# Kernel optimization log

Hardware: AMD Instinct MI355X
Metric: run time of the kernel (lower is better)

## Reference

```python
import jax, jax.numpy as jnp
import numpy as np

D_PET = 128
B = 16


def _mlp(k_vectors, W1, b1, W2, b2, W3, b3):
    # filter_calculator: Linear(3,d) -> silu -> Linear(d,d) -> silu -> Linear(d,d)
    x = jax.nn.silu(jnp.einsum('bkc,cd->bkd', k_vectors, W1) + b1)
    x = jax.nn.silu(jnp.einsum('bkd,de->bke', x, W2) + b2)
    return jnp.einsum('bkd,de->bke', x, W3) + b3


def setup_inputs() -> dict:
    key = jax.random.key(0)
    ks = jax.random.split(key, 10)
    N_B, N_k = 2048, 256
    k_vectors = jax.random.normal(ks[0], (B, N_k, 3), dtype=jnp.float32)
    positions = jax.random.normal(ks[1], (N_B, 3), dtype=jnp.float32)
    h = jax.random.normal(ks[2], (N_B, D_PET), dtype=jnp.float32)
    batch = jnp.sort(jax.random.randint(ks[3], (N_B,), 0, B))
    s3 = 1.0 / np.sqrt(3.0)
    sd = 1.0 / np.sqrt(D_PET)
    W1 = jax.random.uniform(ks[4], (3, D_PET), jnp.float32, -s3, s3)
    b1 = jnp.zeros((D_PET,), jnp.float32)
    W2 = jax.random.uniform(ks[5], (D_PET, D_PET), jnp.float32, -sd, sd)
    b2 = jnp.zeros((D_PET,), jnp.float32)
    W3 = jax.random.uniform(ks[6], (D_PET, D_PET), jnp.float32, -sd, sd)
    b3 = jnp.zeros((D_PET,), jnp.float32)
    return {"k_vectors": k_vectors, "positions": positions, "h": h,
            "W1": W1, "b1": b1, "W2": W2, "b2": b2, "W3": W3, "b3": b3,
            "batch": batch}


def reference(k_vectors, positions, h, W1, b1, W2, b2, W3, b3, batch):
    # gather per-atom k-vectors: [N_B, N_k, 3]
    kv = k_vectors[batch]
    # phase k . r : [N_B, N_k]
    phase = jnp.einsum('nc,nkc->nk', positions, kv)
    ikr = jnp.exp(1j * phase)  # complex64, [N_B, N_k]
    # s = segment-sum over atoms of exp(-i k.r) * h : [B, N_k, d_pet]
    contrib = jnp.conj(ikr)[:, :, None] * h[:, None, :]
    s = jax.ops.segment_sum(contrib, batch, num_segments=B)
    # filter values from k-vectors: [B, N_k, d_pet]
    filt = _mlp(k_vectors, W1, b1, W2, b2, W3, b3)
    # new h: sum over k of exp(i k.r) * s[batch] * filt[batch] : [N_B, d_pet]
    product = ikr[:, :, None] * s[batch] * filt[batch]
    return jnp.sum(product, axis=1)
```

## Files before the change

### kernel.cpp

```cpp
#include <hip/hip_runtime.h>
#include <math.h>

#define D_PET 128
#define NK    256
#define NB    2048
#define NBATCH 16

__device__ __forceinline__ float silu(float x) {
    return x / (1.0f + expf(-x));
}

__device__ __forceinline__ int lower_bound_dev(const int* a, int n, int v) {
    int lo = 0, hi = n;
    while (lo < hi) {
        int m = (lo + hi) >> 1;
        if (a[m] < v) lo = m + 1; else hi = m;
    }
    return lo;
}

#define S_BLOCKS 512
#define MJ 8

#define SLOAD(S, c0)                                                         \
    do {                                                                     \
        _Pragma("unroll")                                                    \
        for (int i_ = 0; i_ < 4; i_++) {                                     \
            int a_ = (c0) * 4 + i_;                                          \
            hb##S[i_] = *(const float4*)(hp + (size_t)(base + a_) * D_PET);  \
            cb##S[i_] = cs[a_ * 8 + kq];                                     \
        }                                                                    \
    } while (0)

#define SFMA(S)                                                              \
    do {                                                                     \
        _Pragma("unroll")                                                    \
        for (int i_ = 0; i_ < 4; i_++) {                                     \
            float4 hv = hb##S[i_]; float2 q = cb##S[i_];                     \
            re[0]=fmaf(q.x,hv.x,re[0]); im[0]=fmaf(-q.y,hv.x,im[0]);         \
            re[1]=fmaf(q.x,hv.y,re[1]); im[1]=fmaf(-q.y,hv.y,im[1]);         \
            re[2]=fmaf(q.x,hv.z,re[2]); im[2]=fmaf(-q.y,hv.z,im[2]);         \
            re[3]=fmaf(q.x,hv.w,re[3]); im[3]=fmaf(-q.y,hv.w,im[3]);         \
        }                                                                    \
    } while (0)

__global__ void __launch_bounds__(256) smlp_kernel(
                           const float* __restrict__ kvec,
                           const float* __restrict__ pos,
                           const float* __restrict__ h,
                           const int* __restrict__ batch,
                           const float* __restrict__ W1, const float* __restrict__ b1,
                           const float* __restrict__ W2, const float* __restrict__ b2,
                           const float* __restrict__ W3, const float* __restrict__ b3,
                           float* __restrict__ filt,
                           float* __restrict__ ts) {
    __shared__ float smem[24 + 2048];

    if (blockIdx.x < S_BLOCKS) {
        int bi = blockIdx.x;
        int v  = (bi & 7) * 64 + (bi >> 3);
        int b  = v >> 5;
        int kt = v & 31;
        int dq = threadIdx.x & 31;
        int kq = threadIdx.x >> 5;
        int k  = kt * 8 + kq;
        int d0 = dq * 4;

        float*  kv_s = smem;
        float2* cs   = (float2*)(smem + 24);

        if (threadIdx.x < 24)
            kv_s[threadIdx.x] = kvec[((size_t)b * NK + kt * 8) * 3 + threadIdx.x];

        int lo = lower_bound_dev(batch, NB, b);
        int hi = lower_bound_dev(batch, NB, b + 1);

        float re[4] = {0.f,0.f,0.f,0.f}, im[4] = {0.f,0.f,0.f,0.f};
        const float* hp = h + d0;

        for (int base = lo; base < hi; base += 128) {
            int m = hi - base; if (m > 128) m = 128;
            __syncthreads();
#pragma unroll
            for (int i = 0; i < 4; i++) {
                int p = threadIdx.x * 4 + i;
                int a = p >> 3, kk = p & 7;
                if (a < m) {
                    int n = base + a;
                    float ph = pos[n*3+0]*kv_s[kk*3+0]
                             + pos[n*3+1]*kv_s[kk*3+1]
                             + pos[n*3+2]*kv_s[kk*3+2];
                    float sv, cv; sincosf(ph, &sv, &cv);
                    cs[a * 8 + kk] = make_float2(cv, sv);
                }
            }
            __syncthreads();

            float4 hb0[4], hb1[4];
            float2 cb0[4], cb1[4];
            int nch = m >> 2;
            if (nch) {
                SLOAD(0, 0);
                int c = 1;
                for (; c + 1 < nch; c += 2) {
                    SLOAD(1, c);     __builtin_amdgcn_sched_barrier(0); SFMA(0);
                    SLOAD(0, c + 1); __builtin_amdgcn_sched_barrier(0); SFMA(1);
                }
                if (c < nch) {
                    SLOAD(1, c); __builtin_amdgcn_sched_barrier(0);
                    SFMA(0); SFMA(1);
                } else {
                    __builtin_amdgcn_sched_barrier(0); SFMA(0);
                }
            }
            for (int a = nch * 4; a < m; a++) {
                float4 hv = *(const float4*)(hp + (size_t)(base + a) * D_PET);
                float2 q  = cs[a * 8 + kq];
                re[0]=fmaf(q.x,hv.x,re[0]); im[0]=fmaf(-q.y,hv.x,im[0]);
                re[1]=fmaf(q.x,hv.y,re[1]); im[1]=fmaf(-q.y,hv.y,im[1]);
                re[2]=fmaf(q.x,hv.z,re[2]); im[2]=fmaf(-q.y,hv.z,im[2]);
                re[3]=fmaf(q.x,hv.w,re[3]); im[3]=fmaf(-q.y,hv.w,im[3]);
            }
        }

        size_t o = (((size_t)b * NK + k) * D_PET + d0) * 2;
        *(float4*)(ts + o)     = make_float4(re[0], im[0], re[1], im[1]);
        *(float4*)(ts + o + 4) = make_float4(re[2], im[2], re[3], im[3]);
        return;
    }

    int bk0 = (blockIdx.x - S_BLOCKS) * MJ;
    int d   = threadIdx.x & (D_PET - 1);
    int jg  = threadIdx.x >> 7;

    float* kv_s  = smem;
    float* x_lds = smem + 24;

    if (threadIdx.x < MJ * 3) kv_s[threadIdx.x] = kvec[bk0 * 3 + threadIdx.x];
    __syncthreads();

    float w10 = W1[0 * D_PET + d], w11 = W1[1 * D_PET + d], w12 = W1[2 * D_PET + d];
    float bb1 = b1[d];
    float4 x1;
    {
        float* xp = (float*)&x1;
#pragma unroll
        for (int i = 0; i < 4; i++) {
            int j = jg * 4 + i;
            float a = bb1;
            a = fmaf(kv_s[j * 3 + 0], w10, a);
            a = fmaf(kv_s[j * 3 + 1], w11, a);
            a = fmaf(kv_s[j * 3 + 2], w12, a);
            xp[i] = silu(a);
        }
    }
    *(float4*)&x_lds[(d << 3) + (jg << 2)] = x1;
    __syncthreads();

    float acc0 = b2[d], acc1 = acc0, acc2 = acc0, acc3 = acc0;
#pragma unroll
    for (int e0 = 0; e0 < D_PET; e0 += 8) {
        float w[8];
#pragma unroll
        for (int i = 0; i < 8; i++) w[i] = W2[(e0 + i) * D_PET + d];
        __builtin_amdgcn_sched_barrier(0);
#pragma unroll
        for (int i = 0; i < 8; i++) {
            float4 xv = *(const float4*)&x_lds[((e0 + i) << 3) + (jg << 2)];
            acc0 = fmaf(xv.x, w[i], acc0);
            acc1 = fmaf(xv.y, w[i], acc1);
            acc2 = fmaf(xv.z, w[i], acc2);
            acc3 = fmaf(xv.w, w[i], acc3);
        }
    }
    float4 x2 = make_float4(silu(acc0), silu(acc1), silu(acc2), silu(acc3));
    __syncthreads();
    *(float4*)&x_lds[(d << 3) + (jg << 2)] = x2;
    __syncthreads();

    float o0 = b3[d], o1 = o0, o2 = o0, o3 = o0;
#pragma unroll
    for (int e0 = 0; e0 < D_PET; e0 += 8) {
        float w[8];
#pragma unroll
        for (int i = 0; i < 8; i++) w[i] = W3[(e0 + i) * D_PET + d];
        __builtin_amdgcn_sched_barrier(0);
#pragma unroll
        for (int i = 0; i < 8; i++) {
            float4 xv = *(const float4*)&x_lds[((e0 + i) << 3) + (jg << 2)];
            o0 = fmaf(xv.x, w[i], o0);
            o1 = fmaf(xv.y, w[i], o1);
            o2 = fmaf(xv.z, w[i], o2);
            o3 = fmaf(xv.w, w[i], o3);
        }
    }
    float out4[4] = {o0, o1, o2, o3};
#pragma unroll
    for (int i = 0; i < 4; i++) {
        int j = jg * 4 + i;
        filt[(size_t)(bk0 + j) * D_PET + d] = out4[i];
    }
}

#define OLOADU(S, c)                                                         \
    do {                                                                     \
        _Pragma("unroll")                                                    \
        for (int j_ = 0; j_ < 2; j_++) {                                     \
            int k_ = k0 + (c) * 2 + j_;                                      \
            t_##S[j_] = *(const float4*)(tb + (size_t)k_ * (2 * D_PET));     \
            f_##S[j_] = *(const float2*)(fb + (size_t)k_ * D_PET);           \
            qA_##S[j_] = csA[k_]; qB_##S[j_] = csB[k_];                      \
        }                                                                    \
    } while (0)

#define OFMAU(S)                                                             \
    do {                                                                     \
        _Pragma("unroll")                                                    \
        for (int j_ = 0; j_ < 2; j_++) {                                     \
            float4 u = t_##S[j_]; float2 f = f_##S[j_];                      \
            float tr0 = u.x*f.x, ti0 = u.y*f.x, tr1 = u.z*f.y, ti1 = u.w*f.y;\
            float2 q = qA_##S[j_];                                           \
            aAr0 = fmaf(q.x,tr0,aAr0); aAr0 = fmaf(-q.y,ti0,aAr0);           \
            aAi0 = fmaf(q.x,ti0,aAi0); aAi0 = fmaf( q.y,tr0,aAi0);           \
            aAr1 = fmaf(q.x,tr1,aAr1); aAr1 = fmaf(-q.y,ti1,aAr1);           \
            aAi1 = fmaf(q.x,ti1,aAi1); aAi1 = fmaf( q.y,tr1,aAi1);           \
            q = qB_##S[j_];                                                  \
            aBr0 = fmaf(q.x,tr0,aBr0); aBr0 = fmaf(-q.y,ti0,aBr0);           \
            aBi0 = fmaf(q.x,ti0,aBi0); aBi0 = fmaf( q.y,tr0,aBi0);           \
            aBr1 = fmaf(q.x,tr1,aBr1); aBr1 = fmaf(-q.y,ti1,aBr1);           \
            aBi1 = fmaf(q.x,ti1,aBi1); aBi1 = fmaf( q.y,tr1,aBi1);           \
        }                                                                    \
    } while (0)

__global__ void __launch_bounds__(512) out_kernel(
                           const float* __restrict__ kvec,
                           const float* __restrict__ pos,
                           const int* __restrict__ batch,
                           const float* __restrict__ ts,
                           const float* __restrict__ filt,
                           float* __restrict__ out, int interleaved) {
    __shared__ float2 cs[4 * 256];
    __shared__ float  red[3][2][64][8];

    int bi = blockIdx.x;
    int v  = (bi & 7) * 64 + (bi >> 3);
    int nb = v * 4;
    int dg = threadIdx.x & 63;
    int w  = threadIdx.x >> 6;
    int ng = w & 1;
    int kh = w >> 1;
    int d0 = dg * 2;
    int k0 = kh * 64;

#pragma unroll
    for (int i = 0; i < 2; i++) {
        int p = threadIdx.x * 2 + i;
        int a = p >> 8, k = p & 255;
        int n = nb + a;
        int b = batch[n];
        const float* kv = kvec + ((size_t)b * NK + k) * 3;
        float ph = pos[n*3+0]*kv[0] + pos[n*3+1]*kv[1] + pos[n*3+2]*kv[2];
        float sv, cv; sincosf(ph, &sv, &cv);
        cs[a * 256 + k] = make_float2(cv, sv);
    }
    __syncthreads();

    int nA = nb + ng * 2, nB = nA + 1;
    int bA = batch[nA], bB = batch[nB];
    const float2* csA = cs + (ng * 2) * 256;
    const float2* csB = csA + 256;

    float aAr0=0.f, aAi0=0.f, aAr1=0.f, aAi1=0.f;
    float aBr0=0.f, aBi0=0.f, aBr1=0.f, aBi1=0.f;

    if (bA == bB) {
        const float* tb = ts   + ((size_t)bA * NK * D_PET + d0) * 2;
        const float* fb = filt +  (size_t)bA * NK * D_PET + d0;

        float4 t_0[2], t_1[2];
        float2 f_0[2], f_1[2];
        float2 qA_0[2], qA_1[2], qB_0[2], qB_1[2];

        OLOADU(0, 0);
#pragma unroll
        for (int c = 1; c + 1 < 32; c += 2) {
            OLOADU(1, c);     __builtin_amdgcn_sched_barrier(0); OFMAU(0);
            OLOADU(0, c + 1); __builtin_amdgcn_sched_barrier(0); OFMAU(1);
        }
        OLOADU(1, 31); __builtin_amdgcn_sched_barrier(0); OFMAU(0); OFMAU(1);
    } else {
        const float* tA = ts   + ((size_t)bA * NK * D_PET + d0) * 2;
        const float* fA = filt +  (size_t)bA * NK * D_PET + d0;
        const float* tB = ts   + ((size_t)bB * NK * D_PET + d0) * 2;
        const float* fB = filt +  (size_t)bB * NK * D_PET + d0;
        for (int k = k0; k < k0 + 64; k++) {
            float4 uA = *(const float4*)(tA + (size_t)k * (2 * D_PET));
            float2 fa = *(const float2*)(fA + (size_t)k * D_PET);
            float4 uB = *(const float4*)(tB + (size_t)k * (2 * D_PET));
            float2 fb2 = *(const float2*)(fB + (size_t)k * D_PET);
            float2 qa = csA[k], qb = csB[k];
            float tr0 = uA.x*fa.x, ti0 = uA.y*fa.x, tr1 = uA.z*fa.y, ti1 = uA.w*fa.y;
            aAr0 = fmaf(qa.x,tr0,aAr0); aAr0 = fmaf(-qa.y,ti0,aAr0);
            aAi0 = fmaf(qa.x,ti0,aAi0); aAi0 = fmaf( qa.y,tr0,aAi0);
            aAr1 = fmaf(qa.x,tr1,aAr1); aAr1 = fmaf(-qa.y,ti1,aAr1);
            aAi1 = fmaf(qa.x,ti1,aAi1); aAi1 = fmaf( qa.y,tr1,aAi1);
            tr0 = uB.x*fb2.x; ti0 = uB.y*fb2.x; tr1 = uB.z*fb2.y; ti1 = uB.w*fb2.y;
            aBr0 = fmaf(qb.x,tr0,aBr0); aBr0 = fmaf(-qb.y,ti0,aBr0);
            aBi0 = fmaf(qb.x,ti0,aBi0); aBi0 = fmaf( qb.y,tr0,aBi0);
            aBr1 = fmaf(qb.x,tr1,aBr1); aBr1 = fmaf(-qb.y,ti1,aBr1);
            aBi1 = fmaf(qb.x,ti1,aBi1); aBi1 = fmaf( qb.y,tr1,aBi1);
        }
    }

    if (kh > 0) {
        float* r = red[kh - 1][ng][dg];
        *(float4*)&r[0] = make_float4(aAr0, aAi0, aAr1, aAi1);
        *(float4*)&r[4] = make_float4(aBr0, aBi0, aBr1, aBi1);
    }
    __syncthreads();
    if (kh == 0) {
#pragma unroll
        for (int q_ = 0; q_ < 3; q_++) {
            const float* r = red[q_][ng][dg];
            aAr0 += r[0]; aAi0 += r[1]; aAr1 += r[2]; aAi1 += r[3];
            aBr0 += r[4]; aBi0 += r[5]; aBr1 += r[6]; aBi1 += r[7];
        }
        if (interleaved) {
            *(float4*)(out + ((size_t)nA * D_PET + d0) * 2) = make_float4(aAr0, aAi0, aAr1, aAi1);
            *(float4*)(out + ((size_t)nB * D_PET + d0) * 2) = make_float4(aBr0, aBi0, aBr1, aBi1);
        } else {
            *(float2*)(out + (size_t)nA * D_PET + d0) = make_float2(aAr0, aAr1);
            *(float2*)(out + (size_t)nB * D_PET + d0) = make_float2(aBr0, aBr1);
        }
    }
}

extern "C" void kernel_launch(void* const* d_in, const int* in_sizes, int n_in,
                              void* d_out, int out_size, void* d_ws, size_t ws_size,
                              hipStream_t stream) {
    const float* kvec = (const float*)d_in[0];
    const float* pos  = (const float*)d_in[1];
    const float* h    = (const float*)d_in[2];
    const float* W1   = (const float*)d_in[3];
    const float* b1   = (const float*)d_in[4];
    const float* W2   = (const float*)d_in[5];
    const float* b2   = (const float*)d_in[6];
    const float* W3   = (const float*)d_in[7];
    const float* b3   = (const float*)d_in[8];
    const int*   batch = (const int*)d_in[9];

    float* ws   = (float*)d_ws;
    float* filt = ws;
    float* ts   = filt + (size_t)NBATCH * NK * D_PET;

    int interleaved = (out_size == NB * D_PET * 2) ? 1 : 0;

    smlp_kernel<<<1024, 256, 0, stream>>>(kvec, pos, h, batch,
                                          W1, b1, W2, b2, W3, b3, filt, ts);
    out_kernel<<<512, 512, 0, stream>>>(kvec, pos, batch, ts, filt,
                                        (float*)d_out, interleaved);
}
```

Before: 119.9 us.

## Split segment-sum atom range in two halves with separate partial buffers

The structure-factor stage now splits each batch's atom range into two halves, handled by separate blocks. This doubles the S-block count to 1024, so the grid gets more parallelism and a shorter per-block reduction loop. Each half writes to its own partial buffer (ts0/ts1), and the output kernel sums the two partials on load. The cost is twice the global reads of the partials in the output kernel, plus an extra workspace buffer.

```diff
diff --git a/kernel.cpp b/kernel.cpp
--- a/kernel.cpp
+++ b/kernel.cpp
@@ -19,7 +19,7 @@
     return lo;
 }
 
-#define S_BLOCKS 512
+#define S_BLOCKS 1024
 #define MJ 8
 
 #define SLOAD(S, c0)                                                         \
@@ -53,14 +53,17 @@
                            const float* __restrict__ W2, const float* __restrict__ b2,
                            const float* __restrict__ W3, const float* __restrict__ b3,
                            float* __restrict__ filt,
-                           float* __restrict__ ts) {
+                           float* __restrict__ ts0,
+                           float* __restrict__ ts1) {
     __shared__ float smem[24 + 2048];
 
     if (blockIdx.x < S_BLOCKS) {
         int bi = blockIdx.x;
-        int v  = (bi & 7) * 64 + (bi >> 3);
-        int b  = v >> 5;
-        int kt = v & 31;
+        int v  = (bi & 7) * 128 + (bi >> 3);
+        int b  = v >> 6;
+        int r  = v & 63;
+        int kt = r >> 1;
+        int sp = r & 1;
         int dq = threadIdx.x & 31;
         int kq = threadIdx.x >> 5;
         int k  = kt * 8 + kq;
@@ -74,12 +77,15 @@
 
         int lo = lower_bound_dev(batch, NB, b);
         int hi = lower_bound_dev(batch, NB, b + 1);
+        int cnt = hi - lo;
+        int a0 = lo + ((cnt * sp) >> 1);
+        int a1 = lo + ((cnt * (sp + 1)) >> 1);
 
         float re[4] = {0.f,0.f,0.f,0.f}, im[4] = {0.f,0.f,0.f,0.f};
         const float* hp = h + d0;
 
-        for (int base = lo; base < hi; base += 128) {
-            int m = hi - base; if (m > 128) m = 128;
+        for (int base = a0; base < a1; base += 128) {
+            int m = a1 - base; if (m > 128) m = 128;
             __syncthreads();
 #pragma unroll
             for (int i = 0; i < 4; i++) {
@@ -123,9 +129,10 @@
             }
         }
 
+        float* dst = sp ? ts1 : ts0;
         size_t o = (((size_t)b * NK + k) * D_PET + d0) * 2;
-        *(float4*)(ts + o)     = make_float4(re[0], im[0], re[1], im[1]);
-        *(float4*)(ts + o + 4) = make_float4(re[2], im[2], re[3], im[3]);
+        *(float4*)(dst + o)     = make_float4(re[0], im[0], re[1], im[1]);
+        *(float4*)(dst + o + 4) = make_float4(re[2], im[2], re[3], im[3]);
         return;
     }
 
@@ -207,8 +214,9 @@
         _Pragma("unroll")                                                    \
         for (int j_ = 0; j_ < 2; j_++) {                                     \
             int k_ = k0 + (c) * 2 + j_;                                      \
-            t_##S[j_] = *(const float4*)(tb + (size_t)k_ * (2 * D_PET));     \
-            f_##S[j_] = *(const float2*)(fb + (size_t)k_ * D_PET);           \
+            t0_##S[j_] = *(const float4*)(tb0 + (size_t)k_ * (2 * D_PET));   \
+            t1_##S[j_] = *(const float4*)(tb1 + (size_t)k_ * (2 * D_PET));   \
+            f_##S[j_]  = *(const float2*)(fb  + (size_t)k_ * D_PET);         \
             qA_##S[j_] = csA[k_]; qB_##S[j_] = csB[k_];                      \
         }                                                                    \
     } while (0)
@@ -217,8 +225,10 @@
     do {                                                                     \
         _Pragma("unroll")                                                    \
         for (int j_ = 0; j_ < 2; j_++) {                                     \
-            float4 u = t_##S[j_]; float2 f = f_##S[j_];                      \
-            float tr0 = u.x*f.x, ti0 = u.y*f.x, tr1 = u.z*f.y, ti1 = u.w*f.y;\
+            float4 u0 = t0_##S[j_], u1 = t1_##S[j_];                         \
+            float2 f = f_##S[j_];                                            \
+            float tr0 = (u0.x + u1.x) * f.x, ti0 = (u0.y + u1.y) * f.x;      \
+            float tr1 = (u0.z + u1.z) * f.y, ti1 = (u0.w + u1.w) * f.y;      \
             float2 q = qA_##S[j_];                                           \
             aAr0 = fmaf(q.x,tr0,aAr0); aAr0 = fmaf(-q.y,ti0,aAr0);           \
             aAi0 = fmaf(q.x,ti0,aAi0); aAi0 = fmaf( q.y,tr0,aAi0);           \
@@ -236,7 +246,8 @@
                            const float* __restrict__ kvec,
                            const float* __restrict__ pos,
                            const int* __restrict__ batch,
-                           const float* __restrict__ ts,
+                           const float* __restrict__ ts0,
+                           const float* __restrict__ ts1,
                            const float* __restrict__ filt,
                            float* __restrict__ out, int interleaved) {
     __shared__ float2 cs[4 * 256];
@@ -274,10 +285,11 @@
     float aBr0=0.f, aBi0=0.f, aBr1=0.f, aBi1=0.f;
 
     if (bA == bB) {
-        const float* tb = ts   + ((size_t)bA * NK * D_PET + d0) * 2;
-        const float* fb = filt +  (size_t)bA * NK * D_PET + d0;
-
-        float4 t_0[2], t_1[2];
+        const float* tb0 = ts0  + ((size_t)bA * NK * D_PET + d0) * 2;
+        const float* tb1 = ts1  + ((size_t)bA * NK * D_PET + d0) * 2;
+        const float* fb  = filt +  (size_t)bA * NK * D_PET + d0;
+
+        float4 t0_0[2], t0_1[2], t1_0[2], t1_1[2];
         float2 f_0[2], f_1[2];
         float2 qA_0[2], qA_1[2], qB_0[2], qB_1[2];
 
@@ -289,22 +301,28 @@
         }
         OLOADU(1, 31); __builtin_amdgcn_sched_barrier(0); OFMAU(0); OFMAU(1);
     } else {
-        const float* tA = ts   + ((size_t)bA * NK * D_PET + d0) * 2;
-        const float* fA = filt +  (size_t)bA * NK * D_PET + d0;
-        const float* tB = ts   + ((size_t)bB * NK * D_PET + d0) * 2;
-        const float* fB = filt +  (size_t)bB * NK * D_PET + d0;
+        const float* tA0 = ts0  + ((size_t)bA * NK * D_PET + d0) * 2;
+        const float* tA1 = ts1  + ((size_t)bA * NK * D_PET + d0) * 2;
+        const float* fA  = filt +  (size_t)bA * NK * D_PET + d0;
+        const float* tB0 = ts0  + ((size_t)bB * NK * D_PET + d0) * 2;
+        const float* tB1 = ts1  + ((size_t)bB * NK * D_PET + d0) * 2;
+        const float* fB  = filt +  (size_t)bB * NK * D_PET + d0;
         for (int k = k0; k < k0 + 64; k++) {
-            float4 uA = *(const float4*)(tA + (size_t)k * (2 * D_PET));
-            float2 fa = *(const float2*)(fA + (size_t)k * D_PET);
-            float4 uB = *(const float4*)(tB + (size_t)k * (2 * D_PET));
-            float2 fb2 = *(const float2*)(fB + (size_t)k * D_PET);
+            float4 uA0 = *(const float4*)(tA0 + (size_t)k * (2 * D_PET));
+            float4 uA1 = *(const float4*)(tA1 + (size_t)k * (2 * D_PET));
+            float2 fa  = *(const float2*)(fA  + (size_t)k * D_PET);
+            float4 uB0 = *(const float4*)(tB0 + (size_t)k * (2 * D_PET));
+            float4 uB1 = *(const float4*)(tB1 + (size_t)k * (2 * D_PET));
+            float2 fb2 = *(const float2*)(fB  + (size_t)k * D_PET);
             float2 qa = csA[k], qb = csB[k];
-            float tr0 = uA.x*fa.x, ti0 = uA.y*fa.x, tr1 = uA.z*fa.y, ti1 = uA.w*fa.y;
+            float tr0 = (uA0.x + uA1.x) * fa.x, ti0 = (uA0.y + uA1.y) * fa.x;
+            float tr1 = (uA0.z + uA1.z) * fa.y, ti1 = (uA0.w + uA1.w) * fa.y;
             aAr0 = fmaf(qa.x,tr0,aAr0); aAr0 = fmaf(-qa.y,ti0,aAr0);
             aAi0 = fmaf(qa.x,ti0,aAi0); aAi0 = fmaf( qa.y,tr0,aAi0);
             aAr1 = fmaf(qa.x,tr1,aAr1); aAr1 = fmaf(-qa.y,ti1,aAr1);
             aAi1 = fmaf(qa.x,ti1,aAi1); aAi1 = fmaf( qa.y,tr1,aAi1);
-            tr0 = uB.x*fb2.x; ti0 = uB.y*fb2.x; tr1 = uB.z*fb2.y; ti1 = uB.w*fb2.y;
+            tr0 = (uB0.x + uB1.x) * fb2.x; ti0 = (uB0.y + uB1.y) * fb2.x;
+            tr1 = (uB0.z + uB1.z) * fb2.y; ti1 = (uB0.w + uB1.w) * fb2.y;
             aBr0 = fmaf(qb.x,tr0,aBr0); aBr0 = fmaf(-qb.y,ti0,aBr0);
             aBi0 = fmaf(qb.x,ti0,aBi0); aBi0 = fmaf( qb.y,tr0,aBi0);
             aBr1 = fmaf(qb.x,tr1,aBr1); aBr1 = fmaf(-qb.y,ti1,aBr1);
@@ -351,12 +369,13 @@
 
     float* ws   = (float*)d_ws;
     float* filt = ws;
-    float* ts   = filt + (size_t)NBATCH * NK * D_PET;
+    float* ts0  = filt + (size_t)NBATCH * NK * D_PET;
+    float* ts1  = ts0 + (size_t)NBATCH * NK * D_PET * 2;
 
     int interleaved = (out_size == NB * D_PET * 2) ? 1 : 0;
 
-    smlp_kernel<<<1024, 256, 0, stream>>>(kvec, pos, h, batch,
-                                          W1, b1, W2, b2, W3, b3, filt, ts);
-    out_kernel<<<512, 512, 0, stream>>>(kvec, pos, batch, ts, filt,
+    smlp_kernel<<<S_BLOCKS + NBATCH * NK / MJ, 256, 0, stream>>>(
+        kvec, pos, h, batch, W1, b1, W2, b2, W3, b3, filt, ts0, ts1);
+    out_kernel<<<512, 512, 0, stream>>>(kvec, pos, batch, ts0, ts1, filt,
                                         (float*)d_out, interleaved);
 }
```

Result: slower. 133.0 us (+10.9%).
